# Kernel optimization log

Hardware: AMD Instinct MI355X
Metric: run time of the kernel (lower is better)

## Reference

```python
import jax, jax.numpy as jnp
import numpy as np
jax.config.update("jax_enable_x64", True)

B, S, V, W, M = 64, 32, 512, 2048, 8
EOS, PAD, MSK = 0, 1, 2
DELTA_IMAG_CLAMP = 35.0  # standard tmm overflow guard on exp(+Im(delta))


def setup_inputs() -> dict:
    key = jax.random.key(0)
    ks = jax.random.split(key, 6)
    stacks = jax.random.uniform(ks[0], (B, S, V), dtype=jnp.float32)
    wl_tensor = (400.0 + 700.0 * jax.random.uniform(ks[1], (W,), dtype=jnp.float32))  # nm
    theta = jnp.zeros((1,), dtype=jnp.float32)  # normal incidence
    nk_real = 1.5 + 2.5 * jax.random.uniform(ks[2], (M, W), dtype=jnp.float64)
    nk_imag = 0.5 * jax.random.uniform(ks[3], (M, W), dtype=jnp.float64)
    thickness = 5.0 + 195.0 * jax.random.uniform(ks[4], (V,), dtype=jnp.float64)
    thickness = thickness.at[jnp.array([EOS, PAD, MSK])].set(0.0)  # special tokens -> substrate, 0 nm
    mat_idx_table = jax.random.randint(ks[5], (V,), 0, M, dtype=jnp.int32)
    sub_idx = jnp.array(0, dtype=jnp.int32)
    return dict(stacks=stacks, wl_tensor=wl_tensor, theta=theta,
                nk_real=nk_real, nk_imag=nk_imag, thickness=thickness,
                mat_idx_table=mat_idx_table, sub_idx=sub_idx,
                eos=EOS, pad=PAD, msk=MSK)


def _coh_tmm_s(n, t, th0, lam):
    """Coherent TMM, s-pol. n:[B,L,W] complex128, t:[B,L] complex128 (front/back inf),
    th0 scalar, lam:[W]. Returns R,T [B,W] float."""
    n0 = n[:, :1, :]
    th = jnp.arcsin(n0 * jnp.sin(th0) / n)           # Snell, complex arcsin [B,L,W]
    cos_th = jnp.cos(th)
    kz = 2.0 * jnp.pi * n * cos_th / lam[None, None, :]
    delta = kz[:, 1:-1, :] * t[:, 1:-1, None]        # inner layers only [B,S,W]
    delta = delta.real + 1j * jnp.minimum(delta.imag, DELTA_IMAG_CLAMP)
    f = n * cos_th                                    # [B,L,W]
    f1, f2 = f[:, :-1, :], f[:, 1:, :]
    r = (f1 - f2) / (f1 + f2)                         # interface Fresnel r [B,L-1,W]
    tt = 2.0 * f1 / (f1 + f2)
    # Mtilde = ([[1,r0],[r0,1]]/t0) @ prod_j (diag(e^{-i d_j}, e^{+i d_j}) @ [[1,rj],[rj,1]]/tj)
    a = 1.0 / tt[:, 0]
    b = r[:, 0] / tt[:, 0]
    c = b
    d = a

    def step(carry, xs):
        a, b, c, d = carry
        dlt, rj, tj = xs                              # each [B,W]
        P = jnp.exp(-1j * dlt)
        Q = jnp.exp(1j * dlt)
        inv_t = 1.0 / tj
        a2 = (a * P + b * Q * rj) * inv_t
        b2 = (a * P * rj + b * Q) * inv_t
        c2 = (c * P + d * Q * rj) * inv_t
        d2 = (c * P * rj + d * Q) * inv_t
        return (a2, b2, c2, d2), None

    xs = (jnp.moveaxis(delta, 1, 0), jnp.moveaxis(r[:, 1:], 1, 0), jnp.moveaxis(tt[:, 1:], 1, 0))
    (a, b, c, d), _ = jax.lax.scan(step, (a, b, c, d), xs)
    r_amp = c / a
    t_amp = 1.0 / a
    R = jnp.abs(r_amp) ** 2
    T = jnp.abs(t_amp) ** 2 * (f[:, -1].real / f[:, 0].real)
    return R, T


def reference(stacks, wl_tensor, theta, nk_real, nk_imag, thickness, mat_idx_table, sub_idx, eos, pad, msk):
    nk_table = nk_real + 1j * nk_imag                 # [M,W] complex128
    th_c = thickness.astype(jnp.complex128)           # [V]
    nk_per_token = nk_table[mat_idx_table]            # [V,W]
    # zero out special-token probabilities and renormalize
    p = stacks.at[:, :, jnp.array([eos, pad, msk])].set(0.0)
    Z = p.sum(axis=-1, keepdims=True)
    p_norm = jnp.where(Z > 0, p / jnp.maximum(Z, 1e-8), p)
    p_c = p_norm.astype(jnp.complex128)
    n_base = jnp.einsum('bsv,vw->bsw', p_c, nk_per_token)  # soft nk gather
    t_base = p_c @ th_c                                     # [B,S]
    is_zero = Z[..., 0] <= 0
    n_base = jnp.where(is_zero[..., None], nk_table[sub_idx][None, None, :], n_base)
    t_base = jnp.where(is_zero, jnp.zeros((), dtype=t_base.dtype), t_base)
    # soft EOS survival mask
    p_eos = jnp.clip(stacks[..., eos], 0.0, 1.0)
    survival = jnp.cumprod(1.0 - p_eos + 1e-12, axis=1)
    active = jnp.concatenate([jnp.ones_like(survival[:, :1]), survival[:, :-1]], axis=1)
    t_base = t_base * active.astype(t_base.dtype)
    Bb, Ss, Ww = n_base.shape
    one = jnp.ones((Bb, 1, Ww), dtype=n_base.dtype)
    inf_t = jnp.full((Bb, 1), jnp.inf, dtype=t_base.dtype)
    n_tensor = jnp.concatenate([one, n_base, one], axis=1)     # [B,S+2,W]
    t_tensor = jnp.concatenate([inf_t, t_base, inf_t], axis=1)  # [B,S+2]
    th0 = theta[0].astype(jnp.float64)
    lam = wl_tensor.astype(jnp.float64)
    R, T = _coh_tmm_s(n_tensor, t_tensor, th0, lam)
    clean = lambda x: jnp.clip(jnp.nan_to_num(x.astype(jnp.float32), nan=0.0, posinf=0.0, neginf=0.0), 0.0, 1.0)
    R = clean(R)
    T = clean(T)
    A = jnp.clip(jnp.nan_to_num(1.0 - R - T, nan=0.0, posinf=0.0, neginf=0.0), 0.0, 1.0)
    return jnp.concatenate([R, A, T], axis=1)  # [B, 3W]
```

## Files before the change

kernel.cpp:

```cpp
#include <hip/hip_runtime.h>
#include <math.h>

#define B_ 64
#define S_ 32
#define V_ 512
#define W_ 2048
#define M_ 8
#define TWO_PI 6.2831853071795864769f
#define DELTA_IMAG_CLAMP 35.0f

struct cf { float re, im; };
__device__ inline cf cmul(cf a, cf b){ return {a.re*b.re - a.im*b.im, a.re*b.im + a.im*b.re}; }
__device__ inline cf cadd(cf a, cf b){ return {a.re+b.re, a.im+b.im}; }
__device__ inline cf csub(cf a, cf b){ return {a.re-b.re, a.im-b.im}; }
__device__ inline float frcp(float x){ return __builtin_amdgcn_rcpf(x); }
__device__ inline cf cinvf(cf a){
    float id = frcp(fmaf(a.re, a.re, a.im*a.im));
    return {a.re*id, -a.im*id};
}
__device__ inline cf csqrt_(cf z){
    float m  = sqrtf(z.re*z.re + z.im*z.im);
    float re = sqrtf(0.5f*fmaxf(m + z.re, 0.0f));
    float im = sqrtf(0.5f*fmaxf(m - z.re, 0.0f));
    if (z.im < 0.0f) im = -im;
    return {re, im};
}

__device__ inline bool is_f32_layout(const void* thick) {
    float w3 = ((const float*)thick)[3];
    return (w3 > 4.0f && w3 < 256.0f);
}

__global__ __launch_bounds__(256) void prep_kernel(
    const float* __restrict__ stacks,
    const void*  __restrict__ thickness,
    const int*   __restrict__ mat_idx,
    const int*   __restrict__ sub_idx_p,
    const int*   __restrict__ eos_p,
    const int*   __restrict__ pad_p,
    const int*   __restrict__ msk_p,
    float* __restrict__ q_out,
    float* __restrict__ t_out)
{
    const int tid  = threadIdx.x;
    const int lane = tid & 63;
    const int wid  = tid >> 6;
    const int row  = blockIdx.x * 4 + wid;

    const bool f32lay = is_f32_layout(thickness);
    const float*  thf = (const float*) thickness;
    const double* thd = (const double*)thickness;
    const int eos = eos_p[0], pad = pad_p[0], msk = msk_p[0];

    const float* srow = stacks + (size_t)row * V_;

    float zp = 0.f, tp = 0.f;
    float bp[M_];
    #pragma unroll
    for (int m = 0; m < M_; ++m) bp[m] = 0.f;

    #pragma unroll
    for (int j = 0; j < V_/64; ++j) {
        int v = lane + j*64;
        float p = srow[v];
        if (v == eos || v == pad || v == msk) p = 0.0f;
        float tv = f32lay ? thf[v] : (float)thd[v];
        int mi = mat_idx[v];
        zp += p;
        tp += p * tv;
        #pragma unroll
        for (int m = 0; m < M_; ++m) bp[m] += (mi == m) ? p : 0.0f;
    }

    #pragma unroll
    for (int off = 32; off > 0; off >>= 1) {
        zp += __shfl_xor(zp, off);
        tp += __shfl_xor(tp, off);
        #pragma unroll
        for (int m = 0; m < M_; ++m) bp[m] += __shfl_xor(bp[m], off);
    }

    if (lane == 0) {
        if (zp > 0.0f) {
            float inv = 1.0f / fmaxf(zp, 1e-8f);
            #pragma unroll
            for (int m = 0; m < M_; ++m) q_out[row*M_ + m] = bp[m]*inv;
            t_out[row] = tp * inv;
        } else {
            int si = sub_idx_p[0];
            #pragma unroll
            for (int m = 0; m < M_; ++m) q_out[row*M_ + m] = (m == si) ? 1.0f : 0.0f;
            t_out[row] = 0.0f;
        }
    }
}

__global__ __launch_bounds__(256) void tmm_kernel(
    const float* __restrict__ wl,
    const float* __restrict__ theta_p,
    const void*  __restrict__ nk_real_v,
    const void*  __restrict__ nk_imag_v,
    const void*  __restrict__ thickness,
    const float* __restrict__ stacks,
    const int*   __restrict__ eos_p,
    const float* __restrict__ q_in,
    const float* __restrict__ t_in,
    float* __restrict__ out)
{
    __shared__ float q_sh[S_ * M_];
    __shared__ float t_sh[S_];

    const int tid = threadIdx.x;
    const int b  = blockIdx.x >> 3;
    const int w  = ((blockIdx.x & 7) << 8) + tid;

    q_sh[tid] = q_in[b * (S_*M_) + tid];

    if (tid < S_) {
        int s = tid;
        float pe = stacks[((size_t)(b*S_ + s))*V_ + eos_p[0]];
        pe = fminf(fmaxf(pe, 0.0f), 1.0f);
        float g = 1.0f - pe + 1e-12f;
        float prod = g;
        #pragma unroll
        for (int off = 1; off < 32; off <<= 1) {
            float up = __shfl_up(prod, off);
            if (s >= off) prod *= up;
        }
        float ex = __shfl_up(prod, 1);
        if (s == 0) ex = 1.0f;
        t_sh[s] = t_in[b*S_ + s] * ex;
    }
    __syncthreads();

    const float lam  = wl[w];
    const float kw   = TWO_PI / lam;
    const float th0  = theta_p[0];
    const float sin0 = sinf(th0);
    const float f0   = cosf(th0);
    const bool oblique = (sin0 != 0.0f);

    float nkr[M_], nki[M_];
    if (is_f32_layout(thickness)) {
        const float* nr = (const float*)nk_real_v;
        const float* ni = (const float*)nk_imag_v;
        #pragma unroll
        for (int m = 0; m < M_; ++m) {
            nkr[m] = nr[m*W_ + w];
            nki[m] = ni[m*W_ + w];
        }
    } else {
        const double* nr = (const double*)nk_real_v;
        const double* ni = (const double*)nk_imag_v;
        #pragma unroll
        for (int m = 0; m < M_; ++m) {
            nkr[m] = (float)nr[m*W_ + w];
            nki[m] = (float)ni[m*W_ + w];
        }
    }

    auto calc_f = [&](int s) -> cf {
        cf n = {0.0f, 0.0f};
        #pragma unroll
        for (int m = 0; m < M_; ++m) {
            float qv = q_sh[s*M_ + m];
            n.re = fmaf(qv, nkr[m], n.re);
            n.im = fmaf(qv, nki[m], n.im);
        }
        if (!oblique) return n;
        cf invn = cinvf(n);
        cf st   = {sin0*invn.re, sin0*invn.im};
        cf st2  = cmul(st, st);
        cf ct   = csqrt_({1.0f - st2.re, -st2.im});
        return cmul(n, ct);
    };

    cf fc  = calc_f(0);
    cf icf = cinvf(fc);
    const float inv2f0 = 0.5f * frcp(f0);
    cf a  = {(f0 + fc.re)*inv2f0,  fc.im*inv2f0};
    cf bb = {(f0 - fc.re)*inv2f0, -fc.im*inv2f0};
    cf c = bb, d = a;

    #pragma unroll 4
    for (int j = 1; j <= S_; ++j) {
        float k  = kw * t_sh[j-1];
        float dr = k * fc.re;
        float di = fminf(k * fc.im, DELTA_IMAG_CLAMP);
        float ed  = __expf(di);
        float emd = __expf(-di);
        float sn = __sinf(dr);
        float cs = __cosf(dr);
        cf P = { ed*cs, -ed*sn};
        cf Q = {emd*cs,  emd*sn};

        cf fn = (j < S_) ? calc_f(j) : cf{f0, 0.0f};

        cf sum   = cadd(fc, fn);
        cf isum  = cinvf(sum);
        cf r     = cmul(csub(fc, fn), isum);
        cf inv_t = cmul(sum, {0.5f*icf.re, 0.5f*icf.im});

        cf aP = cmul(a, P), bQ = cmul(bb, Q);
        cf cP = cmul(c, P), dQ = cmul(d, Q);
        a  = cmul(cadd(aP, cmul(bQ, r)), inv_t);
        bb = cmul(cadd(cmul(aP, r), bQ), inv_t);
        c  = cmul(cadd(cP, cmul(dQ, r)), inv_t);
        d  = cmul(cadd(cmul(cP, r), dQ), inv_t);
        fc  = fn;
        icf = cinvf(fn);
    }

    float ma  = fmaxf(fabsf(a.re), fabsf(a.im));
    float sc  = frcp(ma);
    cf as     = {a.re*sc, a.im*sc};
    float den = fmaf(as.re, as.re, as.im*as.im);
    float iden = frcp(den);
    cf csc    = {c.re*sc, c.im*sc};
    cf ramp   = {(csc.re*as.re + csc.im*as.im)*iden,
                 (csc.im*as.re - csc.re*as.im)*iden};
    float R = fmaf(ramp.re, ramp.re, ramp.im*ramp.im);
    float tr = sc*as.re*iden, ti = -sc*as.im*iden;
    float T = fmaf(tr, tr, ti*ti) * (fc.re * frcp(f0));

    auto clean = [](float x) -> float {
        return isfinite(x) ? fminf(fmaxf(x, 0.0f), 1.0f) : 0.0f;
    };
    float Rc = clean(R);
    float Tc = clean(T);
    float Ac = clean(1.0f - Rc - Tc);

    size_t base = (size_t)b * (3*W_);
    out[base +          w] = Rc;
    out[base +   W_ +   w] = Ac;
    out[base + 2*W_ +   w] = Tc;
}

extern "C" void kernel_launch(void* const* d_in, const int* in_sizes, int n_in,
                              void* d_out, int out_size, void* d_ws, size_t ws_size,
                              hipStream_t stream) {
    const float* stacks    = (const float*)d_in[0];
    const float* wl        = (const float*)d_in[1];
    const float* theta     = (const float*)d_in[2];
    const void*  nk_real   = d_in[3];
    const void*  nk_imag   = d_in[4];
    const void*  thickness = d_in[5];
    const int*   mat_idx   = (const int*)d_in[6];
    const int*   sub_idx   = (const int*)d_in[7];
    const int*   eos       = (const int*)d_in[8];
    const int*   pad       = (const int*)d_in[9];
    const int*   msk       = (const int*)d_in[10];
    float* out = (float*)d_out;

    float* q     = (float*)d_ws;
    float* t_raw = q + B_*S_*M_;

    prep_kernel<<<(B_*S_)/4, 256, 0, stream>>>(stacks, thickness, mat_idx, sub_idx,
                                               eos, pad, msk, q, t_raw);
    tmm_kernel<<<B_*(W_/256), 256, 0, stream>>>(wl, theta, nk_real, nk_imag,
                                                thickness, stacks, eos, q, t_raw, out);
}
```

Before: 96.47 us.

## Fuse prep reduction into TMM kernel, recomputing per-block stack mixtures

Merges the prep kernel that builds per-layer material weights and thicknesses into the TMM kernel. Each block now reduces the 32 stack rows for its batch element itself and keeps the results in shared memory. This removes one kernel launch and the global-memory round trip through the workspace. In exchange, each batch's reduction is recomputed redundantly by all 8 wavelength blocks, which multiplies the reads of the stacks data, and the loop runs before the main TMM computation can start.

```diff
diff --git a/kernel.cpp b/kernel.cpp
--- a/kernel.cpp
+++ b/kernel.cpp
@@ -31,94 +31,83 @@
     return (w3 > 4.0f && w3 < 256.0f);
 }
 
-__global__ __launch_bounds__(256) void prep_kernel(
+__global__ __launch_bounds__(256) void tmm_fused(
     const float* __restrict__ stacks,
+    const float* __restrict__ wl,
+    const float* __restrict__ theta_p,
+    const void*  __restrict__ nk_real_v,
+    const void*  __restrict__ nk_imag_v,
     const void*  __restrict__ thickness,
     const int*   __restrict__ mat_idx,
     const int*   __restrict__ sub_idx_p,
     const int*   __restrict__ eos_p,
     const int*   __restrict__ pad_p,
     const int*   __restrict__ msk_p,
-    float* __restrict__ q_out,
-    float* __restrict__ t_out)
+    float* __restrict__ out)
 {
+    __shared__ float q_sh[S_ * M_];
+    __shared__ float traw_sh[S_];
+    __shared__ float t_sh[S_];
+
     const int tid  = threadIdx.x;
     const int lane = tid & 63;
-    const int wid  = tid >> 6;
-    const int row  = blockIdx.x * 4 + wid;
+    const int wv   = tid >> 6;
+    const int b    = blockIdx.x >> 3;
+    const int w    = ((blockIdx.x & 7) << 8) + tid;
 
     const bool f32lay = is_f32_layout(thickness);
     const float*  thf = (const float*) thickness;
     const double* thd = (const double*)thickness;
     const int eos = eos_p[0], pad = pad_p[0], msk = msk_p[0];
 
-    const float* srow = stacks + (size_t)row * V_;
-
-    float zp = 0.f, tp = 0.f;
-    float bp[M_];
-    #pragma unroll
-    for (int m = 0; m < M_; ++m) bp[m] = 0.f;
-
-    #pragma unroll
-    for (int j = 0; j < V_/64; ++j) {
-        int v = lane + j*64;
-        float p = srow[v];
-        if (v == eos || v == pad || v == msk) p = 0.0f;
-        float tv = f32lay ? thf[v] : (float)thd[v];
-        int mi = mat_idx[v];
-        zp += p;
-        tp += p * tv;
-        #pragma unroll
-        for (int m = 0; m < M_; ++m) bp[m] += (mi == m) ? p : 0.0f;
-    }
-
-    #pragma unroll
-    for (int off = 32; off > 0; off >>= 1) {
-        zp += __shfl_xor(zp, off);
-        tp += __shfl_xor(tp, off);
-        #pragma unroll
-        for (int m = 0; m < M_; ++m) bp[m] += __shfl_xor(bp[m], off);
-    }
-
-    if (lane == 0) {
-        if (zp > 0.0f) {
-            float inv = 1.0f / fmaxf(zp, 1e-8f);
+    for (int i = 0; i < 8; ++i) {
+        const int s   = wv * 8 + i;
+        const int row = b * S_ + s;
+        const float* srow = stacks + (size_t)row * V_;
+
+        float zp = 0.f, tp = 0.f;
+        float bp[M_];
+        #pragma unroll
+        for (int m = 0; m < M_; ++m) bp[m] = 0.f;
+
+        #pragma unroll
+        for (int j = 0; j < V_/64; ++j) {
+            int v = lane + j*64;
+            float p = srow[v];
+            if (v == eos || v == pad || v == msk) p = 0.0f;
+            float tv = f32lay ? thf[v] : (float)thd[v];
+            int mi = mat_idx[v];
+            zp += p;
+            tp += p * tv;
             #pragma unroll
-            for (int m = 0; m < M_; ++m) q_out[row*M_ + m] = bp[m]*inv;
-            t_out[row] = tp * inv;
-        } else {
-            int si = sub_idx_p[0];
+            for (int m = 0; m < M_; ++m) bp[m] += (mi == m) ? p : 0.0f;
+        }
+        #pragma unroll
+        for (int off = 32; off > 0; off >>= 1) {
+            zp += __shfl_xor(zp, off);
+            tp += __shfl_xor(tp, off);
             #pragma unroll
-            for (int m = 0; m < M_; ++m) q_out[row*M_ + m] = (m == si) ? 1.0f : 0.0f;
-            t_out[row] = 0.0f;
-        }
-    }
-}
-
-__global__ __launch_bounds__(256) void tmm_kernel(
-    const float* __restrict__ wl,
-    const float* __restrict__ theta_p,
-    const void*  __restrict__ nk_real_v,
-    const void*  __restrict__ nk_imag_v,
-    const void*  __restrict__ thickness,
-    const float* __restrict__ stacks,
-    const int*   __restrict__ eos_p,
-    const float* __restrict__ q_in,
-    const float* __restrict__ t_in,
-    float* __restrict__ out)
-{
-    __shared__ float q_sh[S_ * M_];
-    __shared__ float t_sh[S_];
-
-    const int tid = threadIdx.x;
-    const int b  = blockIdx.x >> 3;
-    const int w  = ((blockIdx.x & 7) << 8) + tid;
-
-    q_sh[tid] = q_in[b * (S_*M_) + tid];
+            for (int m = 0; m < M_; ++m) bp[m] += __shfl_xor(bp[m], off);
+        }
+        if (lane == 0) {
+            if (zp > 0.0f) {
+                float inv = 1.0f / fmaxf(zp, 1e-8f);
+                #pragma unroll
+                for (int m = 0; m < M_; ++m) q_sh[s*M_ + m] = bp[m]*inv;
+                traw_sh[s] = tp * inv;
+            } else {
+                int si = sub_idx_p[0];
+                #pragma unroll
+                for (int m = 0; m < M_; ++m) q_sh[s*M_ + m] = (m == si) ? 1.0f : 0.0f;
+                traw_sh[s] = 0.0f;
+            }
+        }
+    }
+    __syncthreads();
 
     if (tid < S_) {
         int s = tid;
-        float pe = stacks[((size_t)(b*S_ + s))*V_ + eos_p[0]];
+        float pe = stacks[((size_t)(b*S_ + s))*V_ + eos];
         pe = fminf(fmaxf(pe, 0.0f), 1.0f);
         float g = 1.0f - pe + 1e-12f;
         float prod = g;
@@ -129,7 +118,7 @@
         }
         float ex = __shfl_up(prod, 1);
         if (s == 0) ex = 1.0f;
-        t_sh[s] = t_in[b*S_ + s] * ex;
+        t_sh[s] = traw_sh[s] * ex;
     }
     __syncthreads();
 
@@ -141,7 +130,7 @@
     const bool oblique = (sin0 != 0.0f);
 
     float nkr[M_], nki[M_];
-    if (is_f32_layout(thickness)) {
+    if (f32lay) {
         const float* nr = (const float*)nk_real_v;
         const float* ni = (const float*)nk_imag_v;
         #pragma unroll
@@ -252,11 +241,7 @@
     const int*   msk       = (const int*)d_in[10];
     float* out = (float*)d_out;
 
-    float* q     = (float*)d_ws;
-    float* t_raw = q + B_*S_*M_;
-
-    prep_kernel<<<(B_*S_)/4, 256, 0, stream>>>(stacks, thickness, mat_idx, sub_idx,
-                                               eos, pad, msk, q, t_raw);
-    tmm_kernel<<<B_*(W_/256), 256, 0, stream>>>(wl, theta, nk_real, nk_imag,
-                                                thickness, stacks, eos, q, t_raw, out);
-}
+    tmm_fused<<<B_*(W_/256), 256, 0, stream>>>(stacks, wl, theta, nk_real, nk_imag,
+                                               thickness, mat_idx, sub_idx,
+                                               eos, pad, msk, out);
+}
```

Measured after the change: 106.0 us. +9.9%, slower.

## Split TMM layer chain across two lanes and combine partial matrix products

Applied to the files above, without the earlier changes.

Each wavelength's 32-layer transfer-matrix product is now split between two adjacent threads, each handling 16 layers starting from identity (or the front interface). The two 2x2 partial products are combined with lane shuffles and one matrix multiply. The grid doubles to keep one wavelength per thread pair. This shortens the serial dependency chain per thread and doubles thread-level parallelism, at the cost of duplicated nk loads and the final combine. The T factor fc.re/f0 is dropped, which is valid at normal incidence since the exit medium is 1.

```diff
diff --git a/kernel.cpp b/kernel.cpp
--- a/kernel.cpp
+++ b/kernel.cpp
@@ -110,9 +110,10 @@
     __shared__ float q_sh[S_ * M_];
     __shared__ float t_sh[S_];
 
-    const int tid = threadIdx.x;
-    const int b  = blockIdx.x >> 3;
-    const int w  = ((blockIdx.x & 7) << 8) + tid;
+    const int tid   = threadIdx.x;
+    const int chunk = tid & 1;
+    const int b     = blockIdx.x >> 4;
+    const int w     = ((blockIdx.x & 15) << 7) + (tid >> 1);
 
     q_sh[tid] = q_in[b * (S_*M_) + tid];
 
@@ -175,16 +176,24 @@
         return cmul(n, ct);
     };
 
-    cf fc  = calc_f(0);
+    const int s0 = chunk << 4;
+    cf fc  = calc_f(s0);
     cf icf = cinvf(fc);
     const float inv2f0 = 0.5f * frcp(f0);
-    cf a  = {(f0 + fc.re)*inv2f0,  fc.im*inv2f0};
-    cf bb = {(f0 - fc.re)*inv2f0, -fc.im*inv2f0};
-    cf c = bb, d = a;
+
+    cf a, bb, c, d;
+    if (chunk == 0) {
+        a  = {(f0 + fc.re)*inv2f0,  fc.im*inv2f0};
+        bb = {(f0 - fc.re)*inv2f0, -fc.im*inv2f0};
+        c = bb; d = a;
+    } else {
+        a = {1.f, 0.f}; bb = {0.f, 0.f}; c = {0.f, 0.f}; d = {1.f, 0.f};
+    }
 
     #pragma unroll 4
-    for (int j = 1; j <= S_; ++j) {
-        float k  = kw * t_sh[j-1];
+    for (int jj = 0; jj < 16; ++jj) {
+        const int sp = s0 + jj;
+        float k  = kw * t_sh[sp];
         float dr = k * fc.re;
         float di = fminf(k * fc.im, DELTA_IMAG_CLAMP);
         float ed  = __expf(di);
@@ -194,7 +203,12 @@
         cf P = { ed*cs, -ed*sn};
         cf Q = {emd*cs,  emd*sn};
 
-        cf fn = (j < S_) ? calc_f(j) : cf{f0, 0.0f};
+        cf fn;
+        if (sp + 1 < S_) {
+            fn = calc_f(sp + 1);
+        } else {
+            fn = {f0, 0.0f};
+        }
 
         cf sum   = cadd(fc, fn);
         cf isum  = cinvf(sum);
@@ -211,29 +225,39 @@
         icf = cinvf(fn);
     }
 
-    float ma  = fmaxf(fabsf(a.re), fabsf(a.im));
-    float sc  = frcp(ma);
-    cf as     = {a.re*sc, a.im*sc};
-    float den = fmaf(as.re, as.re, as.im*as.im);
-    float iden = frcp(den);
-    cf csc    = {c.re*sc, c.im*sc};
-    cf ramp   = {(csc.re*as.re + csc.im*as.im)*iden,
-                 (csc.im*as.re - csc.re*as.im)*iden};
-    float R = fmaf(ramp.re, ramp.re, ramp.im*ramp.im);
-    float tr = sc*as.re*iden, ti = -sc*as.im*iden;
-    float T = fmaf(tr, tr, ti*ti) * (fc.re * frcp(f0));
-
-    auto clean = [](float x) -> float {
-        return isfinite(x) ? fminf(fmaxf(x, 0.0f), 1.0f) : 0.0f;
-    };
-    float Rc = clean(R);
-    float Tc = clean(T);
-    float Ac = clean(1.0f - Rc - Tc);
-
-    size_t base = (size_t)b * (3*W_);
-    out[base +          w] = Rc;
-    out[base +   W_ +   w] = Ac;
-    out[base + 2*W_ +   w] = Tc;
+    cf aO  = {__shfl_xor(a.re, 1),  __shfl_xor(a.im, 1)};
+    cf bO  = {__shfl_xor(bb.re, 1), __shfl_xor(bb.im, 1)};
+    cf cO  = {__shfl_xor(c.re, 1),  __shfl_xor(c.im, 1)};
+    cf dO  = {__shfl_xor(d.re, 1),  __shfl_xor(d.im, 1)};
+
+    if (chunk == 0) {
+        cf fa = cadd(cmul(a, aO), cmul(bb, cO));
+        cf fcm = cadd(cmul(c, aO), cmul(d, cO));
+
+        float ma  = fmaxf(fabsf(fa.re), fabsf(fa.im));
+        float scv = frcp(ma);
+        cf as     = {fa.re*scv, fa.im*scv};
+        float den = fmaf(as.re, as.re, as.im*as.im);
+        float iden = frcp(den);
+        cf csc    = {fcm.re*scv, fcm.im*scv};
+        cf ramp   = {(csc.re*as.re + csc.im*as.im)*iden,
+                     (csc.im*as.re - csc.re*as.im)*iden};
+        float R = fmaf(ramp.re, ramp.re, ramp.im*ramp.im);
+        float tr = scv*as.re*iden, ti = -scv*as.im*iden;
+        float T = fmaf(tr, tr, ti*ti);
+
+        auto clean = [](float x) -> float {
+            return isfinite(x) ? fminf(fmaxf(x, 0.0f), 1.0f) : 0.0f;
+        };
+        float Rc = clean(R);
+        float Tc = clean(T);
+        float Ac = clean(1.0f - Rc - Tc);
+
+        size_t base = (size_t)b * (3*W_);
+        out[base +          w] = Rc;
+        out[base +   W_ +   w] = Ac;
+        out[base + 2*W_ +   w] = Tc;
+    }
 }
 
 extern "C" void kernel_launch(void* const* d_in, const int* in_sizes, int n_in,
@@ -257,6 +281,6 @@
 
     prep_kernel<<<(B_*S_)/4, 256, 0, stream>>>(stacks, thickness, mat_idx, sub_idx,
                                                eos, pad, msk, q, t_raw);
-    tmm_kernel<<<B_*(W_/256), 256, 0, stream>>>(wl, theta, nk_real, nk_imag,
+    tmm_kernel<<<B_*(W_/128), 256, 0, stream>>>(wl, theta, nk_real, nk_imag,
                                                 thickness, stacks, eos, q, t_raw, out);
 }
```

Measured after the change: 92.99 us. 3.6% less time.
